# Kernel optimization log

Measured on AMD Instinct MI355X. Metric: run time of the kernel, lower is better.

The kernel has to match this reference:

```python
import jax, jax.numpy as jnp
import numpy as np
import math

D_MODEL = 512
DIM_K = 512
DIM_V = 512
N_HEADS = 8
B, S = 2, 2048


def setup_inputs() -> dict:
    key = jax.random.key(0)
    ks = jax.random.split(key, 10)
    s = 1.0 / math.sqrt(D_MODEL)
    return {
        "x": jax.random.normal(ks[0], (B, S, D_MODEL), jnp.float32),
        "y": jax.random.normal(ks[1], (B, S, D_MODEL), jnp.float32),
        # torch nn.Linear weights: [out, in]
        "q_w": jax.random.normal(ks[2], (DIM_K, D_MODEL), jnp.float32) * s,
        "q_b": jax.random.normal(ks[3], (DIM_K,), jnp.float32) * s,
        "k_w": jax.random.normal(ks[4], (DIM_K, D_MODEL), jnp.float32) * s,
        "k_b": jax.random.normal(ks[5], (DIM_K,), jnp.float32) * s,
        "v_w": jax.random.normal(ks[6], (DIM_V, D_MODEL), jnp.float32) * s,
        "v_b": jax.random.normal(ks[7], (DIM_V,), jnp.float32) * s,
        "o_w": jax.random.normal(ks[8], (D_MODEL, DIM_V), jnp.float32) * s,
        "o_b": jax.random.normal(ks[9], (D_MODEL,), jnp.float32) * s,
    }


def reference(x, y, q_w, q_b, k_w, k_b, v_w, v_b, o_w, o_b):
    b, s, _ = x.shape
    hd_k = DIM_K // N_HEADS
    hd_v = DIM_V // N_HEADS
    norm_fact = 1.0 / math.sqrt(D_MODEL)  # note: original scales by 1/sqrt(d_model)
    # torch code reshapes the flat [B,S,dim] projection row-major into [H,B,S,hd]
    Q = (x @ q_w.T + q_b).reshape(N_HEADS, b, s, hd_k)
    K = (y @ k_w.T + k_b).reshape(N_HEADS, b, s, hd_k)
    V = (y @ v_w.T + v_b).reshape(N_HEADS, b, s, hd_v)
    # scores: [H, B, Sq, Sk]
    scores = jnp.einsum("hbqd,hbkd->hbqk", Q, K) * norm_fact
    # per-row mean threshold: mask (set -inf) where score <= row mean
    thre = jnp.mean(scores, axis=-1, keepdims=True)
    scores = jnp.where(scores <= thre, -jnp.inf, scores)
    attn = jax.nn.softmax(scores, axis=-1)
    out = jnp.einsum("hbqk,hbkd->hbqd", attn, V).reshape(b, s, DIM_V)
    return out @ o_w.T + o_b
```

## Files before the change

### kernel.cpp

```cpp
#include <hip/hip_runtime.h>


typedef unsigned short ushort;
typedef unsigned int uint;

typedef __bf16  bf16x8   __attribute__((ext_vector_type(8)));
typedef float   floatx4  __attribute__((ext_vector_type(4)));
typedef float   floatx16 __attribute__((ext_vector_type(16)));
typedef float   float4v  __attribute__((ext_vector_type(4)));
typedef uint    uint4v   __attribute__((ext_vector_type(4)));
typedef ushort  ushort4v __attribute__((ext_vector_type(4)));

#define MFMA16(a,b,c) __builtin_amdgcn_mfma_f32_16x16x32_bf16((a),(b),(c),0,0,0)
#define MFMA32(a,b,c) __builtin_amdgcn_mfma_f32_32x32x16_bf16((a),(b),(c),0,0,0)

__device__ __forceinline__ float b2f(ushort u){
  union { uint i; float f; } v; v.i = ((uint)u) << 16; return v.f;
}
__device__ __forceinline__ ushort f2b(float f){
  union { float f; uint i; } v; v.f = f;
  uint r = v.i + 0x7FFFu + ((v.i >> 16) & 1u);
  return (ushort)(r >> 16);
}
__device__ __forceinline__ void split2(float f, ushort& h, ushort& l){
  h = f2b(f);
  l = f2b(f - b2f(h));
}
__device__ __forceinline__ void gload16(const ushort* g, ushort* l){
  __builtin_amdgcn_global_load_lds(
      (const __attribute__((address_space(1))) unsigned int*)g,
      (__attribute__((address_space(3))) unsigned int*)l, 16, 0, 0);
}

__global__ __launch_bounds__(256) void split_xy(
    const float* __restrict__ x, const float* __restrict__ y,
    ushort* __restrict__ xhi, ushort* __restrict__ xlo,
    ushort* __restrict__ yhi, ushort* __restrict__ ylo)
{
  int idx = blockIdx.x * 256 + threadIdx.x;
  const float* sp; ushort *hp, *lp; int i;
  if (idx < 524288){ sp = x; hp = xhi; lp = xlo; i = idx; }
  else             { sp = y; hp = yhi; lp = ylo; i = idx - 524288; }
  float4v d = ((const float4v*)sp)[i];
  ushort4v h, l;
  #pragma unroll
  for (int j=0;j<4;j++){ ushort hh,ll; split2(d[j],hh,ll); h[j]=hh; l[j]=ll; }
  ((ushort4v*)hp)[i] = h;
  ((ushort4v*)lp)[i] = l;
}

__global__ __launch_bounds__(256) void split_w(
    const float* __restrict__ qw, const float* __restrict__ kw,
    const float* __restrict__ vw, const float* __restrict__ ow,
    ushort* __restrict__ qwh, ushort* __restrict__ qwl,
    ushort* __restrict__ kwh, ushort* __restrict__ kwl,
    ushort* __restrict__ vwh, ushort* __restrict__ vwl,
    ushort* __restrict__ owh, ushort* __restrict__ owl)
{
  int idx = blockIdx.x * 256 + threadIdx.x;
  int a = idx >> 16, i = idx & 65535;
  const float* sp; ushort *hp, *lp;
  if (a == 0){ sp=qw; hp=qwh; lp=qwl; }
  else if (a == 1){ sp=kw; hp=kwh; lp=kwl; }
  else if (a == 2){ sp=vw; hp=vwh; lp=vwl; }
  else { sp=ow; hp=owh; lp=owl; }
  float4v d = ((const float4v*)sp)[i];
  ushort4v h, l;
  #pragma unroll
  for (int j=0;j<4;j++){ ushort hh,ll; split2(d[j],hh,ll); h[j]=hh; l[j]=ll; }
  ((ushort4v*)hp)[i] = h;
  ((ushort4v*)lp)[i] = l;
}

template<int OUT_MODE, bool KSUM, bool SPLIT_A>
__global__ __launch_bounds__(256) void proj2(
    const ushort* __restrict__ Ahi, const ushort* __restrict__ Alo,
    const ushort* __restrict__ Bhi, const ushort* __restrict__ Blo,
    const float* __restrict__ bias,
    float* __restrict__ outf, ushort* __restrict__ outhi, ushort* __restrict__ outlo,
    float* __restrict__ ksum_out)
{
  const int id = blockIdx.x;
  const int m0 = ((id & 7) * 8 + ((id >> 3) & 7)) * 64;
  const int n0 = (id >> 6) * 64;

  __shared__ __align__(16) ushort AH[2][4096];
  __shared__ __align__(16) ushort AL[SPLIT_A?2:1][4096];
  __shared__ __align__(16) ushort BH[2][4096];
  __shared__ __align__(16) ushort BL[2][4096];
  __shared__ float cs[64];

  const int t    = threadIdx.x;
  const int lane = t & 63;
  const int w    = t >> 6;
  const int wm   = w >> 1, wn = w & 1;
  const int lr   = lane & 15, lg = lane >> 4;

  const int rl  = lane >> 3;
  const int c8s = (lane & 7) ^ rl;
  constexpr int NCH = SPLIT_A ? 8 : 6;

  auto stage = [&](int buf, int k0){
    #pragma unroll
    for (int j = 0; j < NCH; j++){
      const int c = w * NCH + j;
      if (SPLIT_A){
        if (c < 8)
          gload16(Ahi + (size_t)(m0 + c*8 + rl)*512 + k0 + c8s*8, &AH[buf][c*512]);
        else if (c < 16)
          gload16(Alo + (size_t)(m0 + (c-8)*8 + rl)*512 + k0 + c8s*8, &AL[buf][(c-8)*512]);
        else if (c < 24)
          gload16(Bhi + (size_t)(n0 + (c-16)*8 + rl)*512 + k0 + c8s*8, &BH[buf][(c-16)*512]);
        else
          gload16(Blo + (size_t)(n0 + (c-24)*8 + rl)*512 + k0 + c8s*8, &BL[buf][(c-24)*512]);
      } else {
        if (c < 8)
          gload16(Ahi + (size_t)(m0 + c*8 + rl)*512 + k0 + c8s*8, &AH[buf][c*512]);
        else if (c < 16)
          gload16(Bhi + (size_t)(n0 + (c-8)*8 + rl)*512 + k0 + c8s*8, &BH[buf][(c-8)*512]);
        else
          gload16(Blo + (size_t)(n0 + (c-16)*8 + rl)*512 + k0 + c8s*8, &BL[buf][(c-16)*512]);
      }
    }
  };

  floatx4 zf; zf[0]=0.f; zf[1]=0.f; zf[2]=0.f; zf[3]=0.f;
  floatx4 acc[2][2];
  #pragma unroll
  for (int i=0;i<2;i++)
    #pragma unroll
    for (int j=0;j<2;j++) acc[i][j] = zf;

  stage(0, 0);
  __syncthreads();

  int cur = 0;
  for (int it = 0; it < 8; ++it){
    if (it < 7) stage(cur^1, (it+1)*64);

    const ushort* AHc = AH[cur];
    const ushort* ALc = SPLIT_A ? AL[cur] : nullptr;
    const ushort* BHc = BH[cur];
    const ushort* BLc = BL[cur];

    #pragma unroll
    for (int ks=0; ks<2; ks++){
      const int xo = ((ks*4 + lg) ^ (lr & 7)) << 3;
      bf16x8 ah[2], al[2], bh[2], bl[2];
      #pragma unroll
      for (int mi=0;mi<2;mi++){
        const int off = (wm*32 + mi*16 + lr)*64 + xo;
        ah[mi] = *(const bf16x8*)&AHc[off];
        if (SPLIT_A) al[mi] = *(const bf16x8*)&ALc[off];
      }
      #pragma unroll
      for (int ni=0;ni<2;ni++){
        const int off = (wn*32 + ni*16 + lr)*64 + xo;
        bh[ni] = *(const bf16x8*)&BHc[off];
        bl[ni] = *(const bf16x8*)&BLc[off];
      }
      #pragma unroll
      for (int mi=0;mi<2;mi++)
        #pragma unroll
        for (int ni=0;ni<2;ni++){
          acc[mi][ni] = MFMA16(ah[mi], bh[ni], acc[mi][ni]);
          acc[mi][ni] = MFMA16(ah[mi], bl[ni], acc[mi][ni]);
          if (SPLIT_A) acc[mi][ni] = MFMA16(al[mi], bh[ni], acc[mi][ni]);
        }
    }
    __syncthreads();
    cur ^= 1;
  }

  #pragma unroll
  for (int ni=0;ni<2;ni++){
    const int n = n0 + wn*32 + ni*16 + lr;
    const float bn = bias[n];
    #pragma unroll
    for (int mi=0;mi<2;mi++){
      #pragma unroll
      for (int r=0;r<4;r++){
        const int m = m0 + wm*32 + mi*16 + lg*4 + r;
        const float c = acc[mi][ni][r] + bn;
        const size_t off = (size_t)m*512 + n;
        if (OUT_MODE == 0)      { outf[off] = c; }
        else if (OUT_MODE == 1) { ushort h,l; split2(c,h,l); outhi[off]=h; outlo[off]=l; }
        else                    { outhi[off] = f2b(c); }
      }
    }
  }

  if (KSUM) {
    if (t < 64) cs[t] = 0.f;
    __syncthreads();
    #pragma unroll
    for (int ni=0;ni<2;ni++){
      float s = 0.f;
      #pragma unroll
      for (int mi=0;mi<2;mi++)
        #pragma unroll
        for (int r=0;r<4;r++) s += acc[mi][ni][r];
      atomicAdd(&cs[wn*32 + ni*16 + lr], s);
    }
    __syncthreads();
    if (t < 64){
      const int hb = m0 >> 8;
      atomicAdd(&ksum_out[hb*64 + t], cs[t] + 64.f * bias[n0 + t]);
    }
  }
}

__global__ __launch_bounds__(256) void vtrans(
    const ushort* __restrict__ pv, ushort* __restrict__ vt)
{
  const int hb = blockIdx.y;
  const int s0 = blockIdx.x * 64;
  const size_t cb = (size_t)hb * 131072;
  __shared__ __align__(16) ushort T[64][68];
  const int t = threadIdx.x;
  {
    int s = t >> 2, c = (t & 3) * 16;
    *(uint4v*)&T[s][c]     = *(const uint4v*)&pv[cb + (size_t)(s0+s)*64 + c];
    *(uint4v*)&T[s][c + 8] = *(const uint4v*)&pv[cb + (size_t)(s0+s)*64 + c + 8];
  }
  __syncthreads();
  const int d = t >> 2, sc = (t & 3) * 16;
  ushort buf[16];
  #pragma unroll
  for (int i=0;i<16;i++) buf[i] = T[sc + i][d];
  *(uint4v*)&vt[cb + (size_t)d*2048 + s0 + sc]     = *(const uint4v*)&buf[0];
  *(uint4v*)&vt[cb + (size_t)d*2048 + s0 + sc + 8] = *(const uint4v*)&buf[8];
}

__device__ __forceinline__ void stage_tile(
    ushort* khb, ushort* klb, ushort* vtb,
    const ushort* gkhi, const ushort* gklo, const ushort* gvt,
    size_t cb, int kvb, int ws, int l)
{
  const int rsub = l >> 3;
  const int c8   = (l & 7) ^ rsub;
  #pragma unroll
  for (int j = 0; j < 6; j++){
    const int chunk = ws*6 + j;
    const int a   = chunk >> 3;
    const int sub = chunk & 7;
    const int row = sub*8 + rsub;
    if (a == 0)
      gload16(gkhi + cb + (size_t)(kvb + row)*64 + c8*8, khb + sub*512);
    else if (a == 1)
      gload16(gklo + cb + (size_t)(kvb + row)*64 + c8*8, klb + sub*512);
    else
      gload16(gvt  + cb + (size_t)row*2048 + kvb + c8*8, vtb + sub*512);
  }
}

__global__ __launch_bounds__(512) void attn_kernel(
    const ushort* __restrict__ qhi, const ushort* __restrict__ qlo,
    const ushort* __restrict__ khi, const ushort* __restrict__ klo,
    const ushort* __restrict__ vt,  const float* __restrict__ ksum,
    ushort* __restrict__ attno)
{
  const int id = blockIdx.x;
  const int hb = ((id & 7) << 1) | ((id >> 3) & 1);
  const int q0 = (id >> 4) * 128;
  const size_t cb = (size_t)hb * 131072;
  const float C1 = 0.04419417382415922f * 1.44269504088896f;

  __shared__ __align__(16) ushort TILES[2][2][3][4096];

  const int t = threadIdx.x, l = t & 63, w = t >> 6;
  const int half = w >> 2, ws = w & 3;
  const int lq = l & 31, h = l >> 5;
  const int kbase = half * 1024;

  stage_tile(TILES[half][0][0], TILES[half][0][1], TILES[half][0][2],
             khi, klo, vt, cb, kbase, ws, l);

  union U8 { bf16x8 v; ushort u[8]; };
  U8 qfh[4], qfl[4];
  float part = 0.f;
  #pragma unroll
  for (int st=0; st<4; st++){
    size_t g = cb + (size_t)(q0 + ws*32 + lq)*64 + st*16 + h*8;
    qfh[st].v = *(const bf16x8*)&qhi[g];
    qfl[st].v = *(const bf16x8*)&qlo[g];
    float4v k0 = *(const float4v*)&ksum[hb*64 + st*16 + h*8];
    float4v k1 = *(const float4v*)&ksum[hb*64 + st*16 + h*8 + 4];
    #pragma unroll
    for (int j=0;j<4;j++) part += (b2f(qfh[st].u[j])   + b2f(qfl[st].u[j]))   * k0[j];
    #pragma unroll
    for (int j=0;j<4;j++) part += (b2f(qfh[st].u[4+j]) + b2f(qfl[st].u[4+j])) * k1[j];
  }
  part += __shfl_xor(part, 32);
  const float rm = part * (1.f/2048.f);
  const float nrmc = -rm * C1;

  floatx16 O0 = {0,0,0,0,0,0,0,0,0,0,0,0,0,0,0,0};
  floatx16 O1 = O0;
  float za = 0.f, zb = 0.f;

  __syncthreads();

  int cur = 0;
  for (int kt = 0; kt < 16; kt++){
    if (kt + 1 < 16)
      stage_tile(TILES[half][cur^1][0], TILES[half][cur^1][1], TILES[half][cur^1][2],
                 khi, klo, vt, cb, kbase + (kt+1)*64, ws, l);

    const ushort* KHc = TILES[half][cur][0];
    const ushort* KLc = TILES[half][cur][1];
    const ushort* VTc = TILES[half][cur][2];

    floatx16 s0 = {0,0,0,0,0,0,0,0,0,0,0,0,0,0,0,0};
    floatx16 s1 = s0;
    #pragma unroll
    for (int st=0; st<4; st++){
      const int xo = (((st*2 + h) ^ (lq & 7)) << 3);
      bf16x8 kh0 = *(const bf16x8*)&KHc[(lq     )*64 + xo];
      bf16x8 kl0 = *(const bf16x8*)&KLc[(lq     )*64 + xo];
      bf16x8 kh1 = *(const bf16x8*)&KHc[(32 + lq)*64 + xo];
      bf16x8 kl1 = *(const bf16x8*)&KLc[(32 + lq)*64 + xo];
      s0 = MFMA32(kh0, qfh[st].v, s0);
      s1 = MFMA32(kh1, qfh[st].v, s1);
      s0 = MFMA32(kh0, qfl[st].v, s0);
      s1 = MFMA32(kh1, qfl[st].v, s1);
      s0 = MFMA32(kl0, qfh[st].v, s0);
      s1 = MFMA32(kl1, qfh[st].v, s1);
    }

    #pragma unroll
    for (int r=0;r<16;r++){
      float t0 = __builtin_fmaf(s0[r], C1, nrmc);
      float t1 = __builtin_fmaf(s1[r], C1, nrmc);
      float e0 = __builtin_amdgcn_exp2f(t0);
      float e1 = __builtin_amdgcn_exp2f(t1);
      e0 = (t0 > 0.f) ? e0 : 0.f;
      e1 = (t1 > 0.f) ? e1 : 0.f;
      za += e0; zb += e1;
      s0[r] = e0; s1[r] = e1;
    }

    bf16x8 pa[4];
    #pragma unroll
    for (int g=0; g<2; g++){
      const floatx16& sp = g ? s1 : s0;
      #pragma unroll
      for (int sg=0; sg<2; sg++){
        uint X0,X1,X2,X3;
        asm("v_cvt_pk_bf16_f32 %0, %1, %2" : "=v"(X0) : "v"(sp[sg*8+0]), "v"(sp[sg*8+1]));
        asm("v_cvt_pk_bf16_f32 %0, %1, %2" : "=v"(X1) : "v"(sp[sg*8+2]), "v"(sp[sg*8+3]));
        asm("v_cvt_pk_bf16_f32 %0, %1, %2" : "=v"(X2) : "v"(sp[sg*8+4]), "v"(sp[sg*8+5]));
        asm("v_cvt_pk_bf16_f32 %0, %1, %2" : "=v"(X3) : "v"(sp[sg*8+6]), "v"(sp[sg*8+7]));
        asm("v_permlane32_swap_b32 %0, %1" : "+v"(X0), "+v"(X2));
        asm("v_permlane32_swap_b32 %0, %1" : "+v"(X1), "+v"(X3));
        union { uint u[4]; bf16x8 v; } pu;
        pu.u[0]=X0; pu.u[1]=X1; pu.u[2]=X2; pu.u[3]=X3;
        pa[g*2+sg] = pu.v;
      }
    }

    #pragma unroll
    for (int s4=0; s4<4; s4++){
      const int xo = (((s4*2 + h) ^ (lq & 7)) << 3);
      bf16x8 vf0 = *(const bf16x8*)&VTc[(lq     )*64 + xo];
      bf16x8 vf1 = *(const bf16x8*)&VTc[(32 + lq)*64 + xo];
      O0 = MFMA32(pa[s4], vf0, O0);
      O1 = MFMA32(pa[s4], vf1, O1);
    }

    __syncthreads();
    cur ^= 1;
  }

  float zacc = za + zb;
  zacc += __shfl_xor(zacc, 32);
  float* CB = (float*)&TILES[0][0][0][0];
  const int ci = (ws*64 + l)*34;
  if (half == 1){
    #pragma unroll
    for (int i=0;i<16;i++){ CB[ci+i] = O0[i]; CB[ci+16+i] = O1[i]; }
    CB[ci+32] = zacc;
  }
  __syncthreads();
  if (half == 0){
    const float zinv = 1.f / (zacc + CB[ci+32]);
    #pragma unroll
    for (int r=0;r<16;r++){ O0[r] += CB[ci+r]; O1[r] += CB[ci+16+r]; }
    #pragma unroll
    for (int r=0;r<16;r++){
      const int crow = (r&3) + ((r>>2)<<3) + (h<<2);
      const float zi = __shfl(zinv, crow);
      const int q = q0 + ws*32 + crow;
      const size_t base = cb + (size_t)q*64 + lq;
      attno[base]      = f2b(O0[r] * zi);
      attno[base + 32] = f2b(O1[r] * zi);
    }
  }
}

extern "C" void kernel_launch(void* const* d_in, const int* in_sizes, int n_in,
                              void* d_out, int out_size, void* d_ws, size_t ws_size,
                              hipStream_t stream)
{
  const float* x   = (const float*)d_in[0];
  const float* y   = (const float*)d_in[1];
  const float* q_w = (const float*)d_in[2];
  const float* q_b = (const float*)d_in[3];
  const float* k_w = (const float*)d_in[4];
  const float* k_b = (const float*)d_in[5];
  const float* v_w = (const float*)d_in[6];
  const float* v_b = (const float*)d_in[7];
  const float* o_w = (const float*)d_in[8];
  const float* o_b = (const float*)d_in[9];

  const size_t NE = 4096ull * 512;
  const size_t WN = 512ull * 512;
  ushort* p = (ushort*)d_ws;
  ushort* pq_hi = p;
  ushort* pq_lo = pq_hi + NE;
  ushort* pk_hi = pq_lo + NE;
  ushort* pk_lo = pk_hi + NE;
  ushort* pv    = pk_lo + NE;
  ushort* xhi   = pv + NE;
  ushort* xlo   = xhi + NE;
  ushort* yhi   = xlo + NE;
  ushort* ylo   = yhi + NE;
  ushort* vtg   = xhi;
  ushort* attno = xlo;
  ushort* qwh = ylo + NE;
  ushort* qwl = qwh + WN;
  ushort* kwh = qwl + WN;
  ushort* kwl = kwh + WN;
  ushort* vwh = kwl + WN;
  ushort* vwl = vwh + WN;
  ushort* owh = vwl + WN;
  ushort* owl = owh + WN;
  float*  ksumb = (float*)(owl + WN);

  hipMemsetAsync(ksumb, 0, 16 * 64 * sizeof(float), stream);

  split_xy<<<4096, 256, 0, stream>>>(x, y, xhi, xlo, yhi, ylo);
  split_w <<<1024, 256, 0, stream>>>(q_w, k_w, v_w, o_w,
                                     qwh, qwl, kwh, kwl, vwh, vwl, owh, owl);

  proj2<1,false,true ><<<512, 256, 0, stream>>>(xhi, xlo, qwh, qwl, q_b, nullptr, pq_hi, pq_lo, nullptr);
  proj2<1,true ,true ><<<512, 256, 0, stream>>>(yhi, ylo, kwh, kwl, k_b, nullptr, pk_hi, pk_lo, ksumb);
  proj2<2,false,true ><<<512, 256, 0, stream>>>(yhi, ylo, vwh, vwl, v_b, nullptr, pv, nullptr, nullptr);
  vtrans<<<dim3(32,16), 256, 0, stream>>>(pv, vtg);
  attn_kernel<<<256, 512, 0, stream>>>(pq_hi, pq_lo, pk_hi, pk_lo, vtg, ksumb, attno);
  proj2<0,false,false><<<512, 256, 0, stream>>>(attno, nullptr, owh, owl, o_b, (float*)d_out, nullptr, nullptr, nullptr);
}
```

Measured before the change: 109.8 us.

## Split attention keys across two blocks, drop split-precision for V and output projections

The V and output projections now use plain bf16 operands instead of hi/lo split, which removes the low-part weight conversion, staging and extra MFMAs. The attention kernel splits the key range in two across twice as many blocks and writes unnormalised partial outputs plus row sums. A new combine kernel adds the partials and normalises them. The K-low tile is now single-buffered, with an extra barrier per iteration. The changes trade accuracy in the V and output projections, and extra bf16 rounding of the partial outputs, for more parallelism and less projection work.

```diff
diff --git a/kernel.cpp b/kernel.cpp
--- a/kernel.cpp
+++ b/kernel.cpp
@@ -54,25 +54,31 @@
     const float* __restrict__ vw, const float* __restrict__ ow,
     ushort* __restrict__ qwh, ushort* __restrict__ qwl,
     ushort* __restrict__ kwh, ushort* __restrict__ kwl,
-    ushort* __restrict__ vwh, ushort* __restrict__ vwl,
-    ushort* __restrict__ owh, ushort* __restrict__ owl)
+    ushort* __restrict__ vwh, ushort* __restrict__ owh)
 {
   int idx = blockIdx.x * 256 + threadIdx.x;
   int a = idx >> 16, i = idx & 65535;
-  const float* sp; ushort *hp, *lp;
-  if (a == 0){ sp=qw; hp=qwh; lp=qwl; }
-  else if (a == 1){ sp=kw; hp=kwh; lp=kwl; }
-  else if (a == 2){ sp=vw; hp=vwh; lp=vwl; }
-  else { sp=ow; hp=owh; lp=owl; }
-  float4v d = ((const float4v*)sp)[i];
-  ushort4v h, l;
-  #pragma unroll
-  for (int j=0;j<4;j++){ ushort hh,ll; split2(d[j],hh,ll); h[j]=hh; l[j]=ll; }
-  ((ushort4v*)hp)[i] = h;
-  ((ushort4v*)lp)[i] = l;
-}
-
-template<int OUT_MODE, bool KSUM, bool SPLIT_A>
+  if (a < 2){
+    const float* sp = a ? kw : qw;
+    ushort *hp = a ? kwh : qwh, *lp = a ? kwl : qwl;
+    float4v d = ((const float4v*)sp)[i];
+    ushort4v h, l;
+    #pragma unroll
+    for (int j=0;j<4;j++){ ushort hh,ll; split2(d[j],hh,ll); h[j]=hh; l[j]=ll; }
+    ((ushort4v*)hp)[i] = h;
+    ((ushort4v*)lp)[i] = l;
+  } else {
+    const float* sp = (a == 2) ? vw : ow;
+    ushort *hp = (a == 2) ? vwh : owh;
+    float4v d = ((const float4v*)sp)[i];
+    ushort4v h;
+    #pragma unroll
+    for (int j=0;j<4;j++) h[j] = f2b(d[j]);
+    ((ushort4v*)hp)[i] = h;
+  }
+}
+
+template<int OUT_MODE, bool KSUM, int PREC>
 __global__ __launch_bounds__(256) void proj2(
     const ushort* __restrict__ Ahi, const ushort* __restrict__ Alo,
     const ushort* __restrict__ Bhi, const ushort* __restrict__ Blo,
@@ -80,14 +86,15 @@
     float* __restrict__ outf, ushort* __restrict__ outhi, ushort* __restrict__ outlo,
     float* __restrict__ ksum_out)
 {
+  constexpr bool SA = (PREC == 2);
   const int id = blockIdx.x;
   const int m0 = ((id & 7) * 8 + ((id >> 3) & 7)) * 64;
   const int n0 = (id >> 6) * 64;
 
   __shared__ __align__(16) ushort AH[2][4096];
-  __shared__ __align__(16) ushort AL[SPLIT_A?2:1][4096];
+  __shared__ __align__(16) ushort AL[SA?2:1][4096];
   __shared__ __align__(16) ushort BH[2][4096];
-  __shared__ __align__(16) ushort BL[2][4096];
+  __shared__ __align__(16) ushort BL[SA?2:1][4096];
   __shared__ float cs[64];
 
   const int t    = threadIdx.x;
@@ -98,13 +105,13 @@
 
   const int rl  = lane >> 3;
   const int c8s = (lane & 7) ^ rl;
-  constexpr int NCH = SPLIT_A ? 8 : 6;
+  constexpr int NCH = SA ? 8 : 4;
 
   auto stage = [&](int buf, int k0){
     #pragma unroll
     for (int j = 0; j < NCH; j++){
       const int c = w * NCH + j;
-      if (SPLIT_A){
+      if constexpr (SA){
         if (c < 8)
           gload16(Ahi + (size_t)(m0 + c*8 + rl)*512 + k0 + c8s*8, &AH[buf][c*512]);
         else if (c < 16)
@@ -116,10 +123,8 @@
       } else {
         if (c < 8)
           gload16(Ahi + (size_t)(m0 + c*8 + rl)*512 + k0 + c8s*8, &AH[buf][c*512]);
-        else if (c < 16)
+        else
           gload16(Bhi + (size_t)(n0 + (c-8)*8 + rl)*512 + k0 + c8s*8, &BH[buf][(c-8)*512]);
-        else
-          gload16(Blo + (size_t)(n0 + (c-16)*8 + rl)*512 + k0 + c8s*8, &BL[buf][(c-16)*512]);
       }
     }
   };
@@ -139,9 +144,9 @@
     if (it < 7) stage(cur^1, (it+1)*64);
 
     const ushort* AHc = AH[cur];
-    const ushort* ALc = SPLIT_A ? AL[cur] : nullptr;
+    const ushort* ALc = SA ? AL[cur] : nullptr;
     const ushort* BHc = BH[cur];
-    const ushort* BLc = BL[cur];
+    const ushort* BLc = SA ? BL[cur] : nullptr;
 
     #pragma unroll
     for (int ks=0; ks<2; ks++){
@@ -151,21 +156,23 @@
       for (int mi=0;mi<2;mi++){
         const int off = (wm*32 + mi*16 + lr)*64 + xo;
         ah[mi] = *(const bf16x8*)&AHc[off];
-        if (SPLIT_A) al[mi] = *(const bf16x8*)&ALc[off];
+        if constexpr (SA) al[mi] = *(const bf16x8*)&ALc[off];
       }
       #pragma unroll
       for (int ni=0;ni<2;ni++){
         const int off = (wn*32 + ni*16 + lr)*64 + xo;
         bh[ni] = *(const bf16x8*)&BHc[off];
-        bl[ni] = *(const bf16x8*)&BLc[off];
+        if constexpr (SA) bl[ni] = *(const bf16x8*)&BLc[off];
       }
       #pragma unroll
       for (int mi=0;mi<2;mi++)
         #pragma unroll
         for (int ni=0;ni<2;ni++){
           acc[mi][ni] = MFMA16(ah[mi], bh[ni], acc[mi][ni]);
-          acc[mi][ni] = MFMA16(ah[mi], bl[ni], acc[mi][ni]);
-          if (SPLIT_A) acc[mi][ni] = MFMA16(al[mi], bh[ni], acc[mi][ni]);
+          if constexpr (SA){
+            acc[mi][ni] = MFMA16(ah[mi], bl[ni], acc[mi][ni]);
+            acc[mi][ni] = MFMA16(al[mi], bh[ni], acc[mi][ni]);
+          }
         }
     }
     __syncthreads();
@@ -232,25 +239,34 @@
   *(uint4v*)&vt[cb + (size_t)d*2048 + s0 + sc + 8] = *(const uint4v*)&buf[8];
 }
 
-__device__ __forceinline__ void stage_tile(
-    ushort* khb, ushort* klb, ushort* vtb,
-    const ushort* gkhi, const ushort* gklo, const ushort* gvt,
+__device__ __forceinline__ void stage_khvt(
+    ushort* khb, ushort* vtb, const ushort* gkhi, const ushort* gvt,
     size_t cb, int kvb, int ws, int l)
 {
   const int rsub = l >> 3;
   const int c8   = (l & 7) ^ rsub;
   #pragma unroll
-  for (int j = 0; j < 6; j++){
-    const int chunk = ws*6 + j;
+  for (int j = 0; j < 4; j++){
+    const int chunk = ws*4 + j;
     const int a   = chunk >> 3;
     const int sub = chunk & 7;
     const int row = sub*8 + rsub;
     if (a == 0)
       gload16(gkhi + cb + (size_t)(kvb + row)*64 + c8*8, khb + sub*512);
-    else if (a == 1)
-      gload16(gklo + cb + (size_t)(kvb + row)*64 + c8*8, klb + sub*512);
     else
       gload16(gvt  + cb + (size_t)row*2048 + kvb + c8*8, vtb + sub*512);
+  }
+}
+__device__ __forceinline__ void stage_kl(
+    ushort* klb, const ushort* gklo, size_t cb, int kvb, int ws, int l)
+{
+  const int rsub = l >> 3;
+  const int c8   = (l & 7) ^ rsub;
+  #pragma unroll
+  for (int j = 0; j < 2; j++){
+    const int sub = ws*2 + j;
+    const int row = sub*8 + rsub;
+    gload16(gklo + cb + (size_t)(kvb + row)*64 + c8*8, klb + sub*512);
   }
 }
 
@@ -258,23 +274,31 @@
     const ushort* __restrict__ qhi, const ushort* __restrict__ qlo,
     const ushort* __restrict__ khi, const ushort* __restrict__ klo,
     const ushort* __restrict__ vt,  const float* __restrict__ ksum,
-    ushort* __restrict__ attno)
+    ushort* __restrict__ Oa, ushort* __restrict__ Ob,
+    float* __restrict__ za, float* __restrict__ zb)
 {
   const int id = blockIdx.x;
   const int hb = ((id & 7) << 1) | ((id >> 3) & 1);
-  const int q0 = (id >> 4) * 128;
+  const int kv = (id >> 4) & 1;
+  const int q0 = (id >> 5) * 128;
   const size_t cb = (size_t)hb * 131072;
   const float C1 = 0.04419417382415922f * 1.44269504088896f;
 
-  __shared__ __align__(16) ushort TILES[2][2][3][4096];
+  __shared__ __align__(16) ushort SMEM[40960];
+  ushort* KHb = SMEM;
+  ushort* VTb = SMEM + 16384;
+  ushort* KLb = SMEM + 32768;
 
   const int t = threadIdx.x, l = t & 63, w = t >> 6;
   const int half = w >> 2, ws = w & 3;
   const int lq = l & 31, h = l >> 5;
-  const int kbase = half * 1024;
-
-  stage_tile(TILES[half][0][0], TILES[half][0][1], TILES[half][0][2],
-             khi, klo, vt, cb, kbase, ws, l);
+  const int kbase = kv*1024 + half*512;
+
+  ushort* op = kv ? Ob : Oa;
+  float*  zp = kv ? zb : za;
+
+  stage_khvt(KHb + (half*2)*4096, VTb + (half*2)*4096, khi, vt, cb, kbase, ws, l);
+  stage_kl(KLb + half*4096, klo, cb, kbase, ws, l);
 
   union U8 { bf16x8 v; ushort u[8]; };
   U8 qfh[4], qfl[4];
@@ -297,19 +321,19 @@
 
   floatx16 O0 = {0,0,0,0,0,0,0,0,0,0,0,0,0,0,0,0};
   floatx16 O1 = O0;
-  float za = 0.f, zb = 0.f;
+  float za_r = 0.f, zb_r = 0.f;
 
   __syncthreads();
 
-  int cur = 0;
-  for (int kt = 0; kt < 16; kt++){
-    if (kt + 1 < 16)
-      stage_tile(TILES[half][cur^1][0], TILES[half][cur^1][1], TILES[half][cur^1][2],
-                 khi, klo, vt, cb, kbase + (kt+1)*64, ws, l);
-
-    const ushort* KHc = TILES[half][cur][0];
-    const ushort* KLc = TILES[half][cur][1];
-    const ushort* VTc = TILES[half][cur][2];
+  for (int kt = 0; kt < 8; kt++){
+    const int cur = kt & 1;
+    if (kt + 1 < 8)
+      stage_khvt(KHb + (half*2 + (cur^1))*4096, VTb + (half*2 + (cur^1))*4096,
+                 khi, vt, cb, kbase + (kt+1)*64, ws, l);
+
+    const ushort* KHc = KHb + (half*2 + cur)*4096;
+    const ushort* KLc = KLb + half*4096;
+    const ushort* VTc = VTb + (half*2 + cur)*4096;
 
     floatx16 s0 = {0,0,0,0,0,0,0,0,0,0,0,0,0,0,0,0};
     floatx16 s1 = s0;
@@ -327,6 +351,9 @@
       s0 = MFMA32(kl0, qfh[st].v, s0);
       s1 = MFMA32(kl1, qfh[st].v, s1);
     }
+    __syncthreads();
+    if (kt + 1 < 8)
+      stage_kl(KLb + half*4096, klo, cb, kbase + (kt+1)*64, ws, l);
 
     #pragma unroll
     for (int r=0;r<16;r++){
@@ -336,7 +363,7 @@
       float e1 = __builtin_amdgcn_exp2f(t1);
       e0 = (t0 > 0.f) ? e0 : 0.f;
       e1 = (t1 > 0.f) ? e1 : 0.f;
-      za += e0; zb += e1;
+      za_r += e0; zb_r += e1;
       s0[r] = e0; s1[r] = e1;
     }
 
@@ -369,12 +396,11 @@
     }
 
     __syncthreads();
-    cur ^= 1;
-  }
-
-  float zacc = za + zb;
+  }
+
+  float zacc = za_r + zb_r;
   zacc += __shfl_xor(zacc, 32);
-  float* CB = (float*)&TILES[0][0][0][0];
+  float* CB = (float*)SMEM;
   const int ci = (ws*64 + l)*34;
   if (half == 1){
     #pragma unroll
@@ -383,19 +409,39 @@
   }
   __syncthreads();
   if (half == 0){
-    const float zinv = 1.f / (zacc + CB[ci+32]);
+    const float zsum = zacc + CB[ci+32];
+    if (h == 0) zp[hb*2048 + q0 + ws*32 + l] = zsum;
     #pragma unroll
     for (int r=0;r<16;r++){ O0[r] += CB[ci+r]; O1[r] += CB[ci+16+r]; }
     #pragma unroll
     for (int r=0;r<16;r++){
       const int crow = (r&3) + ((r>>2)<<3) + (h<<2);
-      const float zi = __shfl(zinv, crow);
       const int q = q0 + ws*32 + crow;
       const size_t base = cb + (size_t)q*64 + lq;
-      attno[base]      = f2b(O0[r] * zi);
-      attno[base + 32] = f2b(O1[r] * zi);
-    }
-  }
+      op[base]      = f2b(O0[r]);
+      op[base + 32] = f2b(O1[r]);
+    }
+  }
+}
+
+__global__ __launch_bounds__(256) void combine_kernel(
+    const ushort* __restrict__ Oa, const ushort* __restrict__ Ob,
+    const float* __restrict__ za, const float* __restrict__ zb,
+    ushort* __restrict__ attno)
+{
+  const int idx = blockIdx.x * 256 + threadIdx.x;
+  const int q = idx >> 3;
+  const float zi = 1.f / (za[q] + zb[q]);
+  uint4v av = ((const uint4v*)Oa)[idx];
+  uint4v bv = ((const uint4v*)Ob)[idx];
+  uint4v ov;
+  #pragma unroll
+  for (int j=0;j<4;j++){
+    float lo = (b2f((ushort)(av[j] & 0xffff)) + b2f((ushort)(bv[j] & 0xffff))) * zi;
+    float hi = (b2f((ushort)(av[j] >> 16))    + b2f((ushort)(bv[j] >> 16)))    * zi;
+    ov[j] = (uint)f2b(lo) | ((uint)f2b(hi) << 16);
+  }
+  ((uint4v*)attno)[idx] = ov;
 }
 
 extern "C" void kernel_launch(void* const* d_in, const int* in_sizes, int n_in,
@@ -427,26 +473,30 @@
   ushort* ylo   = yhi + NE;
   ushort* vtg   = xhi;
   ushort* attno = xlo;
+  ushort* Oa    = pv;
+  ushort* Ob    = yhi;
+  float*  za    = (float*)ylo;
+  float*  zb    = za + 32768;
   ushort* qwh = ylo + NE;
   ushort* qwl = qwh + WN;
   ushort* kwh = qwl + WN;
   ushort* kwl = kwh + WN;
   ushort* vwh = kwl + WN;
-  ushort* vwl = vwh + WN;
-  ushort* owh = vwl + WN;
-  ushort* owl = owh + WN;
-  float*  ksumb = (float*)(owl + WN);
+  ushort* owh = vwh + WN;
+  float*  ksumb = (float*)(owh + WN);
 
   hipMemsetAsync(ksumb, 0, 16 * 64 * sizeof(float), stream);
 
   split_xy<<<4096, 256, 0, stream>>>(x, y, xhi, xlo, yhi, ylo);
   split_w <<<1024, 256, 0, stream>>>(q_w, k_w, v_w, o_w,
-                                     qwh, qwl, kwh, kwl, vwh, vwl, owh, owl);
-
-  proj2<1,false,true ><<<512, 256, 0, stream>>>(xhi, xlo, qwh, qwl, q_b, nullptr, pq_hi, pq_lo, nullptr);
-  proj2<1,true ,true ><<<512, 256, 0, stream>>>(yhi, ylo, kwh, kwl, k_b, nullptr, pk_hi, pk_lo, ksumb);
-  proj2<2,false,true ><<<512, 256, 0, stream>>>(yhi, ylo, vwh, vwl, v_b, nullptr, pv, nullptr, nullptr);
+                                     qwh, qwl, kwh, kwl, vwh, owh);
+
+  proj2<1,false,2><<<512, 256, 0, stream>>>(xhi, xlo, qwh, qwl, q_b, nullptr, pq_hi, pq_lo, nullptr);
+  proj2<1,true ,2><<<512, 256, 0, stream>>>(yhi, ylo, kwh, kwl, k_b, nullptr, pk_hi, pk_lo, ksumb);
+  proj2<2,false,0><<<512, 256, 0, stream>>>(yhi, nullptr, vwh, nullptr, v_b, nullptr, pv, nullptr, nullptr);
   vtrans<<<dim3(32,16), 256, 0, stream>>>(pv, vtg);
-  attn_kernel<<<256, 512, 0, stream>>>(pq_hi, pq_lo, pk_hi, pk_lo, vtg, ksumb, attno);
-  proj2<0,false,false><<<512, 256, 0, stream>>>(attno, nullptr, owh, owl, o_b, (float*)d_out, nullptr, nullptr, nullptr);
-}
+  attn_kernel<<<512, 512, 0, stream>>>(pq_hi, pq_lo, pk_hi, pk_lo, vtg, ksumb,
+                                       Oa, Ob, za, zb);
+  combine_kernel<<<1024, 256, 0, stream>>>(Oa, Ob, za, zb, attno);
+  proj2<0,false,0><<<512, 256, 0, stream>>>(attno, nullptr, owh, nullptr, o_b, (float*)d_out, nullptr, nullptr, nullptr);
+}
```

Result: no change. 110.7 us (+0.8%).
